# Optimization experiments

Measured on AMD Instinct MI355X. Metric: run time of the kernel, lower is better.

The kernel has to match this reference:

```python
import jax, jax.numpy as jnp
import numpy as np

B, N = 32, 512
N_DIM, N_P, N_K = 128, 3, 2
F0_DIM = N_DIM * N_P            # 384
CAT_DIM = N_DIM * (N_K + 1) * N_P  # 1152


def setup_inputs() -> dict:
    key = jax.random.key(0)
    ks = jax.random.split(key, 12)
    s = 0.05
    return {
        "loc": jax.random.uniform(ks[0], (B, N, 2), dtype=jnp.float32),
        "deadline": jax.random.uniform(ks[1], (B, N), dtype=jnp.float32),
        "workload": jax.random.uniform(ks[2], (B, N), dtype=jnp.float32),
        "depot": jax.random.uniform(ks[3], (B, 1, 2), dtype=jnp.float32),
        "W_init": jax.random.normal(ks[4], (3, F0_DIM), dtype=jnp.float32) * s,
        "b_init": jnp.zeros((F0_DIM,), jnp.float32),
        "W_dep": jax.random.normal(ks[5], (2, N_DIM), dtype=jnp.float32) * s,
        "b_dep": jnp.zeros((N_DIM,), jnp.float32),
        "W_g1": jax.random.normal(ks[6], (CAT_DIM, N_DIM), dtype=jnp.float32) * s,
        "b_g1": jnp.zeros((N_DIM,), jnp.float32),
        "W_g2": jax.random.normal(ks[7], (CAT_DIM, N_DIM), dtype=jnp.float32) * s,
        "b_g2": jnp.zeros((N_DIM,), jnp.float32),
        "W_g3": jax.random.normal(ks[8], (CAT_DIM, N_DIM), dtype=jnp.float32) * s,
        "b_g3": jnp.zeros((N_DIM,), jnp.float32),
        "gamma": jnp.ones((F0_DIM,), jnp.float32),
        "beta": jnp.zeros((F0_DIM,), jnp.float32),
        "W_F": jax.random.normal(ks[9], (F0_DIM, N_DIM), dtype=jnp.float32) * s,
        "b_F": jnp.zeros((N_DIM,), jnp.float32),
    }


def _forward(loc, deadline, workload, depot, W_init, b_init, W_dep, b_dep,
             W_g1, b_g1, W_g2, b_g2, W_g3, b_g3, gamma, beta, W_F, b_F):
    # X = [loc, deadline/deadline.max()] -> [B,N,3] (workload is concatenated then dropped in original)
    X = jnp.concatenate([loc, (deadline / deadline.max())[..., None]], axis=-1)
    n = X.shape[1]
    # pairwise squared distances [B,N,N]
    d2 = ((X[:, :, None, :] - X[:, None, :, :]) ** 2).sum(-1)
    off = ~jnp.eye(n, dtype=bool)                      # off-diagonal mask
    d2_safe = jnp.where(off, d2, 1.0)
    A = jnp.where(off, 1.0 / jnp.sqrt(d2_safe), 0.0)   # A = 1/dist off-diag, 0 on diag
    A = jnp.where(jnp.isnan(A), 0.0, A)                # A[A!=A]=0
    A = A / A.max()                                    # global max-normalize
    deg = A.sum(-1) - 1.0                              # (A.sum(-1) - 1)
    L = jnp.eye(n, dtype=A.dtype) * deg[:, None, :] - A  # D - A (diag = deg)
    L2 = L @ L

    F0 = X @ W_init + b_init                           # [B,N,384]
    F0_sq = F0 * F0
    F0_cu = F0 * F0_sq

    def prop(F):
        return jnp.concatenate([F, L @ F, L2 @ F], axis=-1)  # [B,N,1152]

    g1 = prop(F0) @ W_g1 + b_g1
    g2 = prop(F0_sq) @ W_g2 + b_g2
    g3 = prop(F0_cu) @ W_g3 + b_g3
    F1 = jnp.concatenate([g1, g2, g3], axis=-1)        # [B,N,384]
    F1 = jax.nn.leaky_relu(F1) + F0

    # BatchNorm1d (training mode): stats over flattened (B*N) samples, biased var
    flat = F1.reshape(-1, F1.shape[-1])
    mu = flat.mean(0)
    var = ((flat - mu) ** 2).mean(0)
    F1 = (F1 - mu) / jnp.sqrt(var + 1e-5) * gamma + beta

    F_final = jax.nn.leaky_relu(F1 @ W_F + b_F)        # [B,N,128]
    dep = depot @ W_dep + b_dep                        # [B,1,128]
    h = jnp.concatenate([dep, F_final], axis=1)        # [B,N+1,128]
    return h, h.mean(axis=1)


def reference(loc, deadline, workload, depot, W_init, b_init, W_dep, b_dep,
              W_g1, b_g1, W_g2, b_g2, W_g3, b_g3, gamma, beta, W_F, b_F):
    return _forward(loc, deadline, workload, depot, W_init, b_init, W_dep, b_dep,
                    W_g1, b_g1, W_g2, b_g2, W_g3, b_g3, gamma, beta, W_F, b_F)
```

## Files before the change

kernel.cpp:

```cpp
#include <hip/hip_runtime.h>

#define LEAKY(x) ((x) > 0.0f ? (x) : 0.01f * (x))

typedef __attribute__((ext_vector_type(8))) short bf16x8;
typedef __attribute__((ext_vector_type(4))) float f32x4;
typedef __attribute__((ext_vector_type(8))) unsigned short u16x8;
typedef __attribute__((ext_vector_type(4))) unsigned short u16x4;

__device__ __forceinline__ unsigned short f2bf(float f) {
    unsigned int u = __float_as_uint(f);
    unsigned int r = (u + 0x7fffu + ((u >> 16) & 1u)) >> 16;
    return (unsigned short)r;
}
__device__ __forceinline__ float bf2f(unsigned short u) {
    return __uint_as_float(((unsigned int)u) << 16);
}


__global__ void k_dmax(const float* __restrict__ deadline, float* __restrict__ dmax) {
    __shared__ float red[256];
    int t = threadIdx.x;
    float m = -1e30f;
    for (int i = t; i < 16384; i += 256) m = fmaxf(m, deadline[i]);
    red[t] = m; __syncthreads();
    for (int s = 128; s > 0; s >>= 1) {
        if (t < s) red[t] = fmaxf(red[t], red[t + s]);
        __syncthreads();
    }
    if (t == 0) *dmax = red[0];
}

__global__ __launch_bounds__(256) void k_rowstats(const float* __restrict__ loc,
                                                  const float* __restrict__ deadline,
                                                  const float* __restrict__ dmaxv,
                                                  float* __restrict__ rowsum, float* __restrict__ pmax) {
    int blk = blockIdx.x;
    int wave = threadIdx.x >> 6, lane = threadIdx.x & 63;
    int bi = blk * 4 + wave;
    int b = bi >> 9, i = bi & 511;
    float invd = 1.0f / (*dmaxv);
    const float* lb = loc + b * 1024;
    const float* db = deadline + b * 512;
    float xi = lb[i * 2], yi = lb[i * 2 + 1], zi = db[i] * invd;
    float lsum = 0.f, lmax = 0.f;
    for (int j = lane; j < 512; j += 64) {
        float d0 = xi - lb[j * 2], d1 = yi - lb[j * 2 + 1], d2 = zi - db[j] * invd;
        float dd = d0 * d0 + d1 * d1 + d2 * d2;
        float r = (j == i) ? 0.f : rsqrtf(dd);
        lsum += r; lmax = fmaxf(lmax, r);
    }
    for (int off = 32; off > 0; off >>= 1) {
        lsum += __shfl_down(lsum, off);
        lmax = fmaxf(lmax, __shfl_down(lmax, off));
    }
    __shared__ float smax[4];
    if (lane == 0) { rowsum[bi] = lsum; smax[wave] = lmax; }
    __syncthreads();
    if (threadIdx.x == 0) pmax[blk] = fmaxf(fmaxf(smax[0], smax[1]), fmaxf(smax[2], smax[3]));
}

__global__ void k_amax(const float* __restrict__ pmax, float* __restrict__ amaxf) {
    __shared__ float red[256];
    int t = threadIdx.x;
    float m = 0.f;
    for (int i = t; i < 4096; i += 256) m = fmaxf(m, pmax[i]);
    red[t] = m; __syncthreads();
    for (int s = 128; s > 0; s >>= 1) {
        if (t < s) red[t] = fmaxf(red[t], red[t + s]);
        __syncthreads();
    }
    if (t == 0) *amaxf = red[0];
}

__global__ void k_buildL(const float* __restrict__ loc, const float* __restrict__ deadline,
                         const float* __restrict__ dmaxv, const float* __restrict__ rowsum,
                         const float* __restrict__ amaxf, unsigned short* __restrict__ Lb) {
    int id = blockIdx.x * 256 + threadIdx.x;
    float inv = 1.0f / (*amaxf);
    float invd = 1.0f / (*dmaxv);
    size_t e = (size_t)id * 4;
    size_t bi = e >> 9;
    int b = (int)(bi >> 9);
    int i = (int)(bi & 511);
    int j0 = (int)(e & 511);
    const float* lb = loc + b * 1024;
    const float* db = deadline + b * 512;
    float xi = lb[i * 2], yi = lb[i * 2 + 1], zi = db[i] * invd;
    float4 l01 = *(const float4*)(lb + j0 * 2);
    float4 l23 = *(const float4*)(lb + j0 * 2 + 4);
    float4 dj = *(const float4*)(db + j0);
    float diag = rowsum[bi] * inv - 1.0f;
    float jx[4] = {l01.x, l01.z, l23.x, l23.z};
    float jy[4] = {l01.y, l01.w, l23.y, l23.w};
    float jz[4] = {dj.x * invd, dj.y * invd, dj.z * invd, dj.w * invd};
    u16x4 o;
#pragma unroll
    for (int j = 0; j < 4; j++) {
        float d0 = xi - jx[j], d1 = yi - jy[j], d2 = zi - jz[j];
        float dd = d0 * d0 + d1 * d1 + d2 * d2;
        float v = (i == j0 + j) ? diag : -rsqrtf(dd) * inv;
        o[j] = f2bf(v);
    }
    *(u16x4*)(Lb + e) = o;
}

__global__ void k_F0pow(const float* __restrict__ loc, const float* __restrict__ deadline,
                        const float* __restrict__ dmaxv,
                        const float* __restrict__ Wi, const float* __restrict__ bi_,
                        unsigned short* __restrict__ P1, unsigned short* __restrict__ P2,
                        unsigned short* __restrict__ P3) {
    int id = blockIdx.x * 256 + threadIdx.x;
    int row = id / 96, c4 = (id % 96) * 4;
    float x0 = loc[row * 2], x1 = loc[row * 2 + 1], x2 = deadline[row] / (*dmaxv);
    float4 w0 = *(const float4*)(Wi + c4);
    float4 w1 = *(const float4*)(Wi + 384 + c4);
    float4 w2 = *(const float4*)(Wi + 768 + c4);
    float4 bb = *(const float4*)(bi_ + c4);
    float f[4] = {x0 * w0.x + x1 * w1.x + x2 * w2.x + bb.x,
                  x0 * w0.y + x1 * w1.y + x2 * w2.y + bb.y,
                  x0 * w0.z + x1 * w1.z + x2 * w2.z + bb.z,
                  x0 * w0.w + x1 * w1.w + x2 * w2.w + bb.w};
    u16x4 o1, o2, o3;
#pragma unroll
    for (int j = 0; j < 4; j++) {
        o1[j] = f2bf(f[j]); o2[j] = f2bf(f[j] * f[j]); o3[j] = f2bf(f[j] * f[j] * f[j]);
    }
    size_t e = (size_t)row * 384 + c4;
    *(u16x4*)(P1 + e) = o1; *(u16x4*)(P2 + e) = o2; *(u16x4*)(P3 + e) = o3;
}

__global__ void k_prepW(const float* __restrict__ Wg1, const float* __restrict__ Wg2,
                        const float* __restrict__ Wg3, unsigned short* __restrict__ WgT) {
    int id = blockIdx.x * 256 + threadIdx.x;
    int combo = id / 49152, rem = id % 49152;
    int n = rem / 384, k = rem % 384;
    int kp = combo / 3, part = combo % 3;
    const float* W = (kp == 0) ? Wg1 : (kp == 1 ? Wg2 : Wg3);
    WgT[id] = f2bf(W[(part * 384 + k) * 128 + n]);
}


__device__ __forceinline__ void pipe128x64(
    const unsigned short* __restrict__ A0, int As0, const unsigned short* __restrict__ B0, int Bs0, int it0,
    const unsigned short* __restrict__ A1, int As1, const unsigned short* __restrict__ B1, int Bs1, int it1,
    unsigned short* AsL, unsigned short* BsL,
    f32x4 (&acc)[4][2], int t)
{
    const int lane = t & 63, wave = t >> 6;
    const int wm = wave >> 1, wn = wave & 1;
    const int quad = lane >> 4, l16 = lane & 15;
    const int ra = t >> 1, ca = (t & 1) * 4;
    const int rb = t >> 2, cb = (t & 3) * 2;
    const unsigned short* Ar0 = A0 + (size_t)ra * As0;
    const unsigned short* Ar1 = A1 ? (A1 + (size_t)ra * As1) : Ar0;
    const unsigned short* Br0 = B0 + (size_t)rb * Bs0;
    const unsigned short* Br1 = B1 ? (B1 + (size_t)rb * Bs1) : Br0;
    const int total = it0 + it1;
    u16x8 pa[4], pb[2];
#pragma unroll
    for (int j = 0; j < 4; j++) pa[j] = *(const u16x8*)(Ar0 + (ca + j) * 8);
#pragma unroll
    for (int j = 0; j < 2; j++) pb[j] = *(const u16x8*)(Br0 + (cb + j) * 8);
    int buf = 0;
    for (int s = 0; s < total; s++) {
#pragma unroll
        for (int j = 0; j < 4; j++)
            *(u16x8*)(AsL + buf * 8192 + ra * 64 + (((ca + j) ^ (ra & 7)) * 8)) = pa[j];
#pragma unroll
        for (int j = 0; j < 2; j++)
            *(u16x8*)(BsL + buf * 4096 + rb * 64 + (((cb + j) ^ (rb & 7)) * 8)) = pb[j];
        __syncthreads();
        if (s + 1 < total) {
            int s2 = s + 1;
            int sg = (s2 >= it0);
            int k0 = (sg ? (s2 - it0) : s2) * 64;
            const unsigned short* Ar = sg ? Ar1 : Ar0;
            const unsigned short* Br = sg ? Br1 : Br0;
#pragma unroll
            for (int j = 0; j < 4; j++) pa[j] = *(const u16x8*)(Ar + k0 + (ca + j) * 8);
#pragma unroll
            for (int j = 0; j < 2; j++) pb[j] = *(const u16x8*)(Br + k0 + (cb + j) * 8);
        }
#pragma unroll
        for (int h = 0; h < 2; h++) {
            bf16x8 af[4], bfr[2];
            int phys = ((h * 4 + quad) ^ (l16 & 7)) * 8;
#pragma unroll
            for (int i = 0; i < 4; i++)
                af[i] = *(const bf16x8*)(AsL + buf * 8192 + (wm * 64 + i * 16 + l16) * 64 + phys);
#pragma unroll
            for (int n = 0; n < 2; n++)
                bfr[n] = *(const bf16x8*)(BsL + buf * 4096 + (wn * 32 + n * 16 + l16) * 64 + phys);
#pragma unroll
            for (int i = 0; i < 4; i++)
#pragma unroll
                for (int n = 0; n < 2; n++)
                    acc[i][n] = __builtin_amdgcn_mfma_f32_16x16x32_bf16(af[i], bfr[n], acc[i][n], 0, 0, 0);
        }
        buf ^= 1;
    }
}

__device__ __forceinline__ void pipe64x64(
    const unsigned short* __restrict__ A0, int As0, const unsigned short* __restrict__ B0, int Bs0, int it0,
    unsigned short* AsL, unsigned short* BsL,
    f32x4 (&acc)[2][2], int t)
{
    const int lane = t & 63, wave = t >> 6;
    const int wm = wave >> 1, wn = wave & 1;
    const int quad = lane >> 4, l16 = lane & 15;
    const int rb = t >> 2, cb = (t & 3) * 2;
    const unsigned short* Ar0 = A0 + (size_t)rb * As0;
    const unsigned short* Br0 = B0 + (size_t)rb * Bs0;
    u16x8 pa[2], pb[2];
#pragma unroll
    for (int j = 0; j < 2; j++) { pa[j] = *(const u16x8*)(Ar0 + (cb + j) * 8);
                                  pb[j] = *(const u16x8*)(Br0 + (cb + j) * 8); }
    int buf = 0;
    for (int s = 0; s < it0; s++) {
#pragma unroll
        for (int j = 0; j < 2; j++) {
            int phys = ((cb + j) ^ (rb & 7)) * 8;
            *(u16x8*)(AsL + buf * 4096 + rb * 64 + phys) = pa[j];
            *(u16x8*)(BsL + buf * 4096 + rb * 64 + phys) = pb[j];
        }
        __syncthreads();
        if (s + 1 < it0) {
            int k0 = (s + 1) * 64;
#pragma unroll
            for (int j = 0; j < 2; j++) { pa[j] = *(const u16x8*)(Ar0 + k0 + (cb + j) * 8);
                                          pb[j] = *(const u16x8*)(Br0 + k0 + (cb + j) * 8); }
        }
#pragma unroll
        for (int h = 0; h < 2; h++) {
            bf16x8 af[2], bfr[2];
            int phys = ((h * 4 + quad) ^ (l16 & 7)) * 8;
#pragma unroll
            for (int i = 0; i < 2; i++)
                af[i] = *(const bf16x8*)(AsL + buf * 4096 + (wm * 32 + i * 16 + l16) * 64 + phys);
#pragma unroll
            for (int n = 0; n < 2; n++)
                bfr[n] = *(const bf16x8*)(BsL + buf * 4096 + (wn * 32 + n * 16 + l16) * 64 + phys);
#pragma unroll
            for (int i = 0; i < 2; i++)
#pragma unroll
                for (int n = 0; n < 2; n++)
                    acc[i][n] = __builtin_amdgcn_mfma_f32_16x16x32_bf16(af[i], bfr[n], acc[i][n], 0, 0, 0);
        }
        buf ^= 1;
    }
}

__global__ __launch_bounds__(256) void k_ygemmT(
    const unsigned short* __restrict__ WgT,
    const unsigned short* __restrict__ P1, const unsigned short* __restrict__ P2,
    const unsigned short* __restrict__ P3, unsigned short* __restrict__ Y2T)
{
    __shared__ unsigned short AsL[16384], BsL[8192];
    const int t = threadIdx.x;
    const int id = blockIdx.x;
    const int b = id & 31, tt = id >> 5;
    const int kp = tt >> 3, nb = tt & 7;
    const unsigned short* P = (kp == 0) ? P1 : (kp == 1 ? P2 : P3);
    f32x4 acc[4][2];
#pragma unroll
    for (int i = 0; i < 4; i++)
#pragma unroll
        for (int n = 0; n < 2; n++) acc[i][n] = (f32x4){0.f, 0.f, 0.f, 0.f};
    pipe128x64(WgT + (size_t)(kp * 3 + 2) * 49152, 384,
               P + ((size_t)b * 512 + nb * 64) * 384, 384, 6,
               nullptr, 0, nullptr, 0, 0, AsL, BsL, acc, t);

    const int wave = t >> 6, lane = t & 63;
    const int wm = wave >> 1, wn = wave & 1;
    const int quad = lane >> 4, l16 = lane & 15;
#pragma unroll
    for (int i = 0; i < 4; i++)
#pragma unroll
        for (int n = 0; n < 2; n++) {
            int g = kp * 128 + wm * 64 + i * 16 + quad * 4;
            int node = nb * 64 + wn * 32 + n * 16 + l16;
#pragma unroll
            for (int r = 0; r < 4; r++)
                Y2T[((size_t)b * 384 + g + r) * 512 + node] = f2bf(acc[i][n][r]);
        }
}

__global__ __launch_bounds__(256) void k_lg1T(
    const unsigned short* __restrict__ Lb, const unsigned short* __restrict__ Y2T,
    const unsigned short* __restrict__ WgT,
    const unsigned short* __restrict__ P1, const unsigned short* __restrict__ P2,
    const unsigned short* __restrict__ P3, unsigned short* __restrict__ ZT)
{
    __shared__ unsigned short AsL[16384], BsL[8192];
    const int t = threadIdx.x;
    const int id = blockIdx.x;
    const int b = id & 31, tt = id >> 5;
    const int kp = tt >> 3, nb = tt & 7;
    const unsigned short* P = (kp == 0) ? P1 : (kp == 1 ? P2 : P3);
    f32x4 acc[4][2];
#pragma unroll
    for (int i = 0; i < 4; i++)
#pragma unroll
        for (int n = 0; n < 2; n++) acc[i][n] = (f32x4){0.f, 0.f, 0.f, 0.f};
    pipe128x64(Y2T + (size_t)b * 196608 + (size_t)kp * 128 * 512, 512,
               Lb + (size_t)b * 262144 + (size_t)nb * 64 * 512, 512, 8,
               WgT + (size_t)(kp * 3 + 1) * 49152, 384,
               P + ((size_t)b * 512 + nb * 64) * 384, 384, 6, AsL, BsL, acc, t);

    const int wave = t >> 6, lane = t & 63;
    const int wm = wave >> 1, wn = wave & 1;
    const int quad = lane >> 4, l16 = lane & 15;
#pragma unroll
    for (int i = 0; i < 4; i++)
#pragma unroll
        for (int n = 0; n < 2; n++) {
            int g = kp * 128 + wm * 64 + i * 16 + quad * 4;
            int node = nb * 64 + wn * 32 + n * 16 + l16;
#pragma unroll
            for (int r = 0; r < 4; r++)
                ZT[((size_t)b * 384 + g + r) * 512 + node] = f2bf(acc[i][n][r]);
        }
}

__global__ __launch_bounds__(256) void k_lg2(
    const unsigned short* __restrict__ Lb, const unsigned short* __restrict__ ZT,
    const unsigned short* __restrict__ WgT,
    const unsigned short* __restrict__ P1, const unsigned short* __restrict__ P2,
    const unsigned short* __restrict__ P3,
    const float* __restrict__ bg1, const float* __restrict__ bg2, const float* __restrict__ bg3,
    unsigned short* __restrict__ F1b, float* __restrict__ bn1, float* __restrict__ bn2)
{
    __shared__ unsigned short AsL[16384], BsL[8192];
    __shared__ float bnS[64], bnQ[64];
    const int t = threadIdx.x;
    const int id = blockIdx.x;
    const int b = id & 31, tt = id >> 5;
    const int mb = tt & 3, gt = tt >> 2;
    const int kp = gt >> 1;
    if (t < 64) { bnS[t] = 0.f; bnQ[t] = 0.f; }
    const unsigned short* P = (kp == 0) ? P1 : (kp == 1 ? P2 : P3);
    f32x4 acc[4][2];
#pragma unroll
    for (int i = 0; i < 4; i++)
#pragma unroll
        for (int n = 0; n < 2; n++) acc[i][n] = (f32x4){0.f, 0.f, 0.f, 0.f};
    pipe128x64(Lb + (size_t)b * 262144 + (size_t)mb * 128 * 512, 512,
               ZT + (size_t)b * 196608 + (size_t)gt * 64 * 512, 512, 8,
               P + ((size_t)b * 512 + mb * 128) * 384, 384,
               WgT + (size_t)(kp * 3) * 49152 + (size_t)(gt & 1) * 64 * 384, 384, 6,
               AsL, BsL, acc, t);

    const int wave = t >> 6, lane = t & 63;
    const int wm = wave >> 1, wn = wave & 1;
    const int quad = lane >> 4, l16 = lane & 15;
    const float* bg = (kp == 0) ? bg1 : (kp == 1 ? bg2 : bg3);
    float ls1[2], ls2[2];
#pragma unroll
    for (int n = 0; n < 2; n++) { ls1[n] = 0.f; ls2[n] = 0.f; }
#pragma unroll
    for (int i = 0; i < 4; i++) {
        int rowl = mb * 128 + wm * 64 + i * 16 + quad * 4;
        size_t rowg = (size_t)b * 512 + rowl;
#pragma unroll
        for (int n = 0; n < 2; n++) {
            int nloc = wn * 32 + n * 16 + l16;
            int g = gt * 64 + nloc;
            float bias = bg[(gt & 1) * 64 + nloc];
#pragma unroll
            for (int r = 0; r < 4; r++) {
                size_t idx = (rowg + r) * 384 + g;
                float c = acc[i][n][r] + bias;
                float v = LEAKY(c) + bf2f(P1[idx]);
                F1b[idx] = f2bf(v);
                ls1[n] += v; ls2[n] += v * v;
            }
        }
    }
#pragma unroll
    for (int n = 0; n < 2; n++) {
        int nloc = wn * 32 + n * 16 + l16;
        atomicAdd(&bnS[nloc], ls1[n]);
        atomicAdd(&bnQ[nloc], ls2[n]);
    }
    __syncthreads();
    if (t < 64) {
        atomicAdd(&bn1[gt * 64 + t], bnS[t]);
        atomicAdd(&bn2[gt * 64 + t], bnQ[t]);
    }
}

__global__ __launch_bounds__(384) void k_bnfin_beff(
    const float* __restrict__ bn1, const float* __restrict__ bn2,
    const float* __restrict__ gamma, const float* __restrict__ beta,
    const float* __restrict__ WF, const float* __restrict__ bF,
    float* __restrict__ sS, float* __restrict__ beffv)
{
    __shared__ float ttL[384];
    int c = threadIdx.x;
    float mu = bn1[c] * (1.f / 16384.f);
    float var = bn2[c] * (1.f / 16384.f) - mu * mu;
    float sc = gamma[c] / sqrtf(var + 1e-5f);
    sS[c] = sc;
    ttL[c] = beta[c] - mu * sc;
    __syncthreads();
    if (c < 128) {
        float a = bF[c];
        for (int k = 0; k < 384; k++) a += ttL[k] * WF[k * 128 + c];
        beffv[c] = a;
    }
}

__global__ void k_fold(const float* __restrict__ WF, const float* __restrict__ sS,
                       unsigned short* __restrict__ WFsT) {
    int id = blockIdx.x * 256 + threadIdx.x;
    int n = id / 384, k = id % 384;
    WFsT[id] = f2bf(WF[k * 128 + n] * sS[k]);
}

__global__ __launch_bounds__(256) void k_fgemm(
    const unsigned short* __restrict__ F1b, const unsigned short* __restrict__ WFsT,
    const float* __restrict__ beffv, float* __restrict__ out, float* __restrict__ msum)
{
    __shared__ unsigned short AsL[8192], BsL[8192];
    __shared__ float msS[64];
    const int t = threadIdx.x;
    const int id = blockIdx.x;
    const int b = id & 31, tt = id >> 5;
    const int seg = tt >> 1, nt = tt & 1;
    if (t < 64) msS[t] = 0.f;
    f32x4 acc[2][2];
#pragma unroll
    for (int i = 0; i < 2; i++)
#pragma unroll
        for (int n = 0; n < 2; n++) acc[i][n] = (f32x4){0.f, 0.f, 0.f, 0.f};
    pipe64x64(F1b + ((size_t)b * 512 + seg * 64) * 384, 384,
              WFsT + (size_t)nt * 64 * 384, 384, 6, AsL, BsL, acc, t);

    const int wave = t >> 6, lane = t & 63;
    const int wm = wave >> 1, wn = wave & 1;
    const int quad = lane >> 4, l16 = lane & 15;
    float ls[2];
#pragma unroll
    for (int n = 0; n < 2; n++) ls[n] = 0.f;
#pragma unroll
    for (int i = 0; i < 2; i++) {
        int nd = seg * 64 + wm * 32 + i * 16 + quad * 4;
#pragma unroll
        for (int n = 0; n < 2; n++) {
            int col = nt * 64 + wn * 32 + n * 16 + l16;
            float bb = beffv[col];
#pragma unroll
            for (int r = 0; r < 4; r++) {
                float x = acc[i][n][r] + bb;
                float v = LEAKY(x);
                out[(size_t)b * 65664 + (size_t)(nd + r + 1) * 128 + col] = v;
                ls[n] += v;
            }
        }
    }
#pragma unroll
    for (int n = 0; n < 2; n++) atomicAdd(&msS[wn * 32 + n * 16 + l16], ls[n]);
    __syncthreads();
    if (t < 64) atomicAdd(&msum[b * 128 + nt * 64 + t], msS[t]);
}

__global__ void k_meandep(const float* __restrict__ depot, const float* __restrict__ Wd,
                          const float* __restrict__ bd, const float* __restrict__ msum,
                          float* __restrict__ out) {
    int id = blockIdx.x * 256 + threadIdx.x;
    int b = id >> 7, o = id & 127;
    float dep = depot[b * 2] * Wd[o] + depot[b * 2 + 1] * Wd[128 + o] + bd[o];
    out[(size_t)b * 65664 + o] = dep;
    out[2101248 + id] = (msum[id] + dep) * (1.0f / 513.0f);
}


extern "C" void kernel_launch(void* const* d_in, const int* in_sizes, int n_in,
                              void* d_out, int out_size, void* d_ws, size_t ws_size,
                              hipStream_t stream) {
    const float* loc      = (const float*)d_in[0];
    const float* deadline = (const float*)d_in[1];
    const float* depot    = (const float*)d_in[3];
    const float* W_init   = (const float*)d_in[4];
    const float* b_init   = (const float*)d_in[5];
    const float* W_dep    = (const float*)d_in[6];
    const float* b_dep    = (const float*)d_in[7];
    const float* W_g1     = (const float*)d_in[8];
    const float* b_g1     = (const float*)d_in[9];
    const float* W_g2     = (const float*)d_in[10];
    const float* b_g2     = (const float*)d_in[11];
    const float* W_g3     = (const float*)d_in[12];
    const float* b_g3     = (const float*)d_in[13];
    const float* gamma    = (const float*)d_in[14];
    const float* beta     = (const float*)d_in[15];
    const float* W_F      = (const float*)d_in[16];
    const float* b_F      = (const float*)d_in[17];
    float* out = (float*)d_out;
    float* ws  = (float*)d_ws;

    float* dmaxv  = ws + 0;
    float* amaxf  = ws + 4;
    float* bn1    = ws + 8;
    float* bn2    = ws + 392;
    float* msum   = ws + 776;
    float* rowsum = ws + 4872;
    float* pmax   = ws + 21256;
    float* sS     = ws + 25352;
    float* beffv  = ws + 25736;
    unsigned short* Lb   = (unsigned short*)(ws + 25864);
    unsigned short* P1   = (unsigned short*)(ws + 4220168);
    unsigned short* P2   = (unsigned short*)(ws + 7365896);
    unsigned short* P3   = (unsigned short*)(ws + 10511624);
    unsigned short* WgT  = (unsigned short*)(ws + 13657352);
    unsigned short* WFsT = (unsigned short*)(ws + 13878536);
    unsigned short* Y2T  = (unsigned short*)(ws + 13903112);
    unsigned short* ZT   = (unsigned short*)(ws + 17048840);
    unsigned short* F1b  = (unsigned short*)(ws + 20194568);

    hipMemsetAsync(bn1, 0, (384 + 384 + 4096) * sizeof(float), stream);

    k_dmax<<<1, 256, 0, stream>>>(deadline, dmaxv);
    k_rowstats<<<4096, 256, 0, stream>>>(loc, deadline, dmaxv, rowsum, pmax);
    k_amax<<<1, 256, 0, stream>>>(pmax, amaxf);
    k_buildL<<<8192, 256, 0, stream>>>(loc, deadline, dmaxv, rowsum, amaxf, Lb);
    k_F0pow<<<6144, 256, 0, stream>>>(loc, deadline, dmaxv, W_init, b_init, P1, P2, P3);
    k_prepW<<<1728, 256, 0, stream>>>(W_g1, W_g2, W_g3, WgT);

    k_ygemmT<<<768, 256, 0, stream>>>(WgT, P1, P2, P3, Y2T);
    k_lg1T<<<768, 256, 0, stream>>>(Lb, Y2T, WgT, P1, P2, P3, ZT);
    k_lg2<<<768, 256, 0, stream>>>(Lb, ZT, WgT, P1, P2, P3,
                                   b_g1, b_g2, b_g3, F1b, bn1, bn2);

    k_bnfin_beff<<<1, 384, 0, stream>>>(bn1, bn2, gamma, beta, W_F, b_F, sS, beffv);
    k_fold<<<192, 256, 0, stream>>>(W_F, sS, WFsT);
    k_fgemm<<<512, 256, 0, stream>>>(F1b, WFsT, beffv, out, msum);
    k_meandep<<<16, 256, 0, stream>>>(depot, W_dep, b_dep, msum, out);
}
```

Baseline: 236.9 us.

## Deepen GEMM global prefetch to two register stages and reorder block mapping

The shared bf16 MFMA GEMM helpers now hold two register stages of global loads, so each tile is fetched two iterations ahead instead of one. The main loop is unrolled by two and alternates between the two register sets, which gives more time to hide global memory latency behind the MFMA work. Separately, the Y-GEMM, LG1 and LG2 kernels change how the block index maps to tile coordinates: the polynomial/group index now varies fastest, so neighbouring blocks share input rows, which may improve cache reuse. The cost is extra VGPRs for the second prefetch set, which could lower occupancy. The unroll by two also assumes an even iteration count.

Result: slower. 244.2 us (+3.1%).

```diff
diff --git a/kernel.cpp b/kernel.cpp
--- a/kernel.cpp
+++ b/kernel.cpp
@@ -156,47 +156,61 @@
     const unsigned short* Br0 = B0 + (size_t)rb * Bs0;
     const unsigned short* Br1 = B1 ? (B1 + (size_t)rb * Bs1) : Br0;
     const int total = it0 + it1;
-    u16x8 pa[4], pb[2];
-#pragma unroll
-    for (int j = 0; j < 4; j++) pa[j] = *(const u16x8*)(Ar0 + (ca + j) * 8);
-#pragma unroll
-    for (int j = 0; j < 2; j++) pb[j] = *(const u16x8*)(Br0 + (cb + j) * 8);
-    int buf = 0;
-    for (int s = 0; s < total; s++) {
+
+    u16x8 paA[4], pbA[2], paB[4], pbB[2];
+
+    auto loadStage = [&](int idx, u16x8 (&pa)[4], u16x8 (&pb)[2]) {
+        int sg = (idx >= it0);
+        int k0 = (sg ? idx - it0 : idx) * 64;
+        const unsigned short* Ar = sg ? Ar1 : Ar0;
+        const unsigned short* Br = sg ? Br1 : Br0;
+#pragma unroll
+        for (int j = 0; j < 4; j++) pa[j] = *(const u16x8*)(Ar + k0 + (ca + j) * 8);
+#pragma unroll
+        for (int j = 0; j < 2; j++) pb[j] = *(const u16x8*)(Br + k0 + (cb + j) * 8);
+    };
+    auto writeStage = [&](int bf_, u16x8 (&pa)[4], u16x8 (&pb)[2]) {
 #pragma unroll
         for (int j = 0; j < 4; j++)
-            *(u16x8*)(AsL + buf * 8192 + ra * 64 + (((ca + j) ^ (ra & 7)) * 8)) = pa[j];
+            *(u16x8*)(AsL + bf_ * 8192 + ra * 64 + (((ca + j) ^ (ra & 7)) * 8)) = pa[j];
 #pragma unroll
         for (int j = 0; j < 2; j++)
-            *(u16x8*)(BsL + buf * 4096 + rb * 64 + (((cb + j) ^ (rb & 7)) * 8)) = pb[j];
-        __syncthreads();
-        if (s + 1 < total) {
-            int s2 = s + 1;
-            int sg = (s2 >= it0);
-            int k0 = (sg ? (s2 - it0) : s2) * 64;
-            const unsigned short* Ar = sg ? Ar1 : Ar0;
-            const unsigned short* Br = sg ? Br1 : Br0;
-#pragma unroll
-            for (int j = 0; j < 4; j++) pa[j] = *(const u16x8*)(Ar + k0 + (ca + j) * 8);
-#pragma unroll
-            for (int j = 0; j < 2; j++) pb[j] = *(const u16x8*)(Br + k0 + (cb + j) * 8);
-        }
+            *(u16x8*)(BsL + bf_ * 4096 + rb * 64 + (((cb + j) ^ (rb & 7)) * 8)) = pb[j];
+    };
+    auto mfmaStep = [&](int bf_) {
 #pragma unroll
         for (int h = 0; h < 2; h++) {
             bf16x8 af[4], bfr[2];
             int phys = ((h * 4 + quad) ^ (l16 & 7)) * 8;
 #pragma unroll
             for (int i = 0; i < 4; i++)
-                af[i] = *(const bf16x8*)(AsL + buf * 8192 + (wm * 64 + i * 16 + l16) * 64 + phys);
+                af[i] = *(const bf16x8*)(AsL + bf_ * 8192 + (wm * 64 + i * 16 + l16) * 64 + phys);
 #pragma unroll
             for (int n = 0; n < 2; n++)
-                bfr[n] = *(const bf16x8*)(BsL + buf * 4096 + (wn * 32 + n * 16 + l16) * 64 + phys);
+                bfr[n] = *(const bf16x8*)(BsL + bf_ * 4096 + (wn * 32 + n * 16 + l16) * 64 + phys);
 #pragma unroll
             for (int i = 0; i < 4; i++)
 #pragma unroll
                 for (int n = 0; n < 2; n++)
                     acc[i][n] = __builtin_amdgcn_mfma_f32_16x16x32_bf16(af[i], bfr[n], acc[i][n], 0, 0, 0);
         }
+    };
+
+    loadStage(0, paA, pbA);
+    loadStage(1, paB, pbB);
+
+    int buf = 0;
+    for (int s = 0; s < total; s += 2) {
+        writeStage(buf, paA, pbA);
+        __syncthreads();
+        if (s + 2 < total) loadStage(s + 2, paA, pbA);
+        mfmaStep(buf);
+        buf ^= 1;
+
+        writeStage(buf, paB, pbB);
+        __syncthreads();
+        if (s + 3 < total) loadStage(s + 3, paB, pbB);
+        mfmaStep(buf);
         buf ^= 1;
     }
 }
@@ -212,41 +226,54 @@
     const int rb = t >> 2, cb = (t & 3) * 2;
     const unsigned short* Ar0 = A0 + (size_t)rb * As0;
     const unsigned short* Br0 = B0 + (size_t)rb * Bs0;
-    u16x8 pa[2], pb[2];
-#pragma unroll
-    for (int j = 0; j < 2; j++) { pa[j] = *(const u16x8*)(Ar0 + (cb + j) * 8);
-                                  pb[j] = *(const u16x8*)(Br0 + (cb + j) * 8); }
-    int buf = 0;
-    for (int s = 0; s < it0; s++) {
+
+    u16x8 paA[2], pbA[2], paB[2], pbB[2];
+    auto loadStage = [&](int idx, u16x8 (&pa)[2], u16x8 (&pb)[2]) {
+        int k0 = idx * 64;
+#pragma unroll
+        for (int j = 0; j < 2; j++) { pa[j] = *(const u16x8*)(Ar0 + k0 + (cb + j) * 8);
+                                      pb[j] = *(const u16x8*)(Br0 + k0 + (cb + j) * 8); }
+    };
+    auto writeStage = [&](int bf_, u16x8 (&pa)[2], u16x8 (&pb)[2]) {
 #pragma unroll
         for (int j = 0; j < 2; j++) {
             int phys = ((cb + j) ^ (rb & 7)) * 8;
-            *(u16x8*)(AsL + buf * 4096 + rb * 64 + phys) = pa[j];
-            *(u16x8*)(BsL + buf * 4096 + rb * 64 + phys) = pb[j];
-        }
-        __syncthreads();
-        if (s + 1 < it0) {
-            int k0 = (s + 1) * 64;
-#pragma unroll
-            for (int j = 0; j < 2; j++) { pa[j] = *(const u16x8*)(Ar0 + k0 + (cb + j) * 8);
-                                          pb[j] = *(const u16x8*)(Br0 + k0 + (cb + j) * 8); }
-        }
+            *(u16x8*)(AsL + bf_ * 4096 + rb * 64 + phys) = pa[j];
+            *(u16x8*)(BsL + bf_ * 4096 + rb * 64 + phys) = pb[j];
+        }
+    };
+    auto mfmaStep = [&](int bf_) {
 #pragma unroll
         for (int h = 0; h < 2; h++) {
             bf16x8 af[2], bfr[2];
             int phys = ((h * 4 + quad) ^ (l16 & 7)) * 8;
 #pragma unroll
             for (int i = 0; i < 2; i++)
-                af[i] = *(const bf16x8*)(AsL + buf * 4096 + (wm * 32 + i * 16 + l16) * 64 + phys);
+                af[i] = *(const bf16x8*)(AsL + bf_ * 4096 + (wm * 32 + i * 16 + l16) * 64 + phys);
 #pragma unroll
             for (int n = 0; n < 2; n++)
-                bfr[n] = *(const bf16x8*)(BsL + buf * 4096 + (wn * 32 + n * 16 + l16) * 64 + phys);
+                bfr[n] = *(const bf16x8*)(BsL + bf_ * 4096 + (wn * 32 + n * 16 + l16) * 64 + phys);
 #pragma unroll
             for (int i = 0; i < 2; i++)
 #pragma unroll
                 for (int n = 0; n < 2; n++)
                     acc[i][n] = __builtin_amdgcn_mfma_f32_16x16x32_bf16(af[i], bfr[n], acc[i][n], 0, 0, 0);
         }
+    };
+
+    loadStage(0, paA, pbA);
+    loadStage(1, paB, pbB);
+    int buf = 0;
+    for (int s = 0; s < it0; s += 2) {
+        writeStage(buf, paA, pbA);
+        __syncthreads();
+        if (s + 2 < it0) loadStage(s + 2, paA, pbA);
+        mfmaStep(buf);
+        buf ^= 1;
+        writeStage(buf, paB, pbB);
+        __syncthreads();
+        if (s + 3 < it0) loadStage(s + 3, paB, pbB);
+        mfmaStep(buf);
         buf ^= 1;
     }
 }
@@ -260,7 +287,7 @@
     const int t = threadIdx.x;
     const int id = blockIdx.x;
     const int b = id & 31, tt = id >> 5;
-    const int kp = tt >> 3, nb = tt & 7;
+    const int kp = tt % 3, nb = tt / 3;
     const unsigned short* P = (kp == 0) ? P1 : (kp == 1 ? P2 : P3);
     f32x4 acc[4][2];
 #pragma unroll
@@ -296,7 +323,7 @@
     const int t = threadIdx.x;
     const int id = blockIdx.x;
     const int b = id & 31, tt = id >> 5;
-    const int kp = tt >> 3, nb = tt & 7;
+    const int kp = tt % 3, nb = tt / 3;
     const unsigned short* P = (kp == 0) ? P1 : (kp == 1 ? P2 : P3);
     f32x4 acc[4][2];
 #pragma unroll
@@ -336,7 +363,7 @@
     const int t = threadIdx.x;
     const int id = blockIdx.x;
     const int b = id & 31, tt = id >> 5;
-    const int mb = tt & 3, gt = tt >> 2;
+    const int gt = tt % 6, mb = tt / 6;
     const int kp = gt >> 1;
     if (t < 64) { bnS[t] = 0.f; bnQ[t] = 0.f; }
     const unsigned short* P = (kp == 0) ? P1 : (kp == 1 ? P2 : P3);
```
